# Performance work log

Measured on AMD Instinct MI355X. Metric: run time of the kernel, lower is better.

The kernel has to match this reference:

```python
import jax, jax.numpy as jnp
import numpy as np

N = 16000; E = 256000; K = 4000; H = 4; D = 128; CL = 16
NODE_VOCAB = 512; TASK_VOCAB = 128; NEG = 0.2


def _gat_sparse(h_in, src, dst, W, a_s, a_d, b):
    # PyG GATConv, heads=H, concat=False, eval mode (attention dropout off)
    n = h_in.shape[0]
    h = (h_in @ W.T).reshape(n, H, D)                       # [N,H,D]
    e = jax.nn.leaky_relu((h * a_s).sum(-1)[src] + (h * a_d).sum(-1)[dst], NEG)  # [E,H]
    emax = jax.ops.segment_max(e, dst, num_segments=n)
    ex = jnp.exp(e - emax[dst])
    den = jax.ops.segment_sum(ex, dst, num_segments=n)
    alpha = ex / (den[dst] + 1e-16)                         # edge softmax over dst
    out = jax.ops.segment_sum(h[src] * alpha[:, :, None], dst, num_segments=n)
    return out.mean(axis=1) + b                             # mean over heads + bias


def reference(x, edge_index, batch, task, node_emb, task_emb,
              W1, as1, ad1, b1, W2, as2, ad2, b2, W3, as3, ad3, b3,
              sag_wrel, sag_brel, sag_wroot, dmon_w, dmon_b,
              Wt, att_s_t, att_d_t, bt, gate_w, gate_b, trans_w, trans_b,
              task_w, task_b, fuse_w, fuse_b, out_w, out_b):
    src0, dst0 = edge_index[0], edge_index[1]
    loops = jnp.arange(N, dtype=src0.dtype)                 # GATConv add_self_loops=True
    src = jnp.concatenate([src0, loops]); dst = jnp.concatenate([dst0, loops])
    h = node_emb[x]
    h = jax.nn.relu(_gat_sparse(h, src, dst, W1, as1, ad1, b1))
    h = jax.nn.relu(_gat_sparse(h, src, dst, W2, as2, ad2, b2))
    h = jax.nn.relu(_gat_sparse(h, src, dst, W3, as3, ad3, b3))
    # SAGPooling: GraphConv score (add-aggr) + top-k (single graph, k=K), tanh gating
    agg = jax.ops.segment_sum(h[src0], dst0, num_segments=N)
    score = (agg @ sag_wrel.T + sag_brel + h @ sag_wroot.T)[:, 0]
    vals, perm = jax.lax.top_k(score, K)
    xp = h[perm] * jnp.tanh(vals)[:, None]                  # [K,D]
    # filter_adj + to_dense_adj: dense [K,K] adjacency among kept nodes (adj[src,dst]+=1)
    new_idx = jnp.full((N,), -1, jnp.int32).at[perm].set(jnp.arange(K, dtype=jnp.int32))
    ni, nj = new_idx[src0], new_idx[dst0]
    valid = (ni >= 0) & (nj >= 0)
    adj = jnp.zeros((K + 1, K + 1), xp.dtype).at[
        jnp.where(valid, ni, K), jnp.where(valid, nj, K)].add(1.0)[:K, :K]
    dx, adj = xp[None], adj[None]                           # [1,K,D], [1,K,K]; mask all-true
    # DMoNPooling
    s = jax.nn.softmax(dx @ dmon_w.T + dmon_b, axis=-1)     # [1,K,CL]
    out_x = jax.nn.selu(jnp.einsum('bnc,bnf->bcf', s, dx))  # [1,CL,D]
    out_adj = jnp.einsum('bnc,bnm,bmd->bcd', s, adj, s)     # [1,CL,CL]
    deg = adj.sum(axis=1)[..., None]                        # einsum('ijk->ik'): [1,K,1]
    m = deg.sum(axis=(1, 2)) / 2
    ca = jnp.einsum('bnc,bnl->bcl', s, deg)                 # [1,CL,1]
    cb = jnp.einsum('bln,bnc->blc', jnp.swapaxes(deg, 1, 2), s)  # [1,1,CL]
    spectral = (-jnp.trace(out_adj - ca @ cb / 2 / m[:, None, None], axis1=1, axis2=2) / 2 / m).mean()
    ss = jnp.einsum('bnc,bnd->bcd', s, s)
    i_s = jnp.eye(CL, dtype=ss.dtype)
    ortho = jnp.linalg.norm(ss / jnp.linalg.norm(ss, axis=(1, 2), keepdims=True)
                            - i_s / jnp.sqrt(jnp.asarray(CL, ss.dtype)), axis=(1, 2)).mean()
    cluster = (jnp.linalg.norm(s.sum(axis=1), axis=1) / K * jnp.sqrt(jnp.asarray(CL, ss.dtype)) - 1).mean()
    gp_loss = spectral + ortho + cluster
    out_adj = out_adj * (1.0 - i_s)                         # zero diagonal
    ds = jnp.sqrt(out_adj.sum(axis=2)) + 1e-15              # [1,CL]
    out_adj = out_adj / ds[:, None, :] / ds[:, :, None]
    # DenseGATConv (add_loop=True sets diag to 1; adj only used as a mask)
    hh = (out_x @ Wt.T).reshape(1, CL, H, D)
    al = jax.nn.leaky_relu((hh * att_s_t).sum(-1)[:, None, :, :]
                           + (hh * att_d_t).sum(-1)[:, :, None, :], NEG)  # [1,i,j,H]
    adj_l = out_adj * (1.0 - i_s) + i_s
    al = jnp.where(adj_l[..., None] == 0, -jnp.inf, al)
    al = jax.nn.softmax(al, axis=2)
    dg = jax.nn.relu(jnp.einsum('bijh,bjhd->bihd', al, hh).mean(axis=2) + bt)  # [1,CL,D]
    # gated readout (DenseAggregation)
    gate = jax.nn.softmax((dg @ gate_w.T + gate_b)[..., 0], axis=-1)           # [1,CL]
    ro = jnp.einsum('bn,bnd->bd', gate, dg @ trans_w.T + trans_b)              # [1,D]
    te = jax.nn.relu(task_emb[task] @ task_w.T + task_b)                       # [1,D]
    fuse = jax.nn.relu(jnp.concatenate([ro, te], axis=-1) @ fuse_w.T + fuse_b)
    out = fuse @ out_w.T + out_b                                               # [1,1]
    return out, gp_loss


def setup_inputs() -> dict:
    key = jax.random.key(0)
    ks = iter(jax.random.split(key, 64))
    def nrm(shape, scale=0.05):
        return jax.random.normal(next(ks), shape, jnp.float32) * scale
    inp = {}
    inp['x'] = jax.random.randint(next(ks), (N,), 0, NODE_VOCAB, dtype=jnp.int32)
    src = jax.random.randint(next(ks), (E,), 0, N, dtype=jnp.int32)
    off = jax.random.randint(next(ks), (E,), 1, N, dtype=jnp.int32)
    inp['edge_index'] = jnp.stack([src, (src + off) % N])  # no self-loops
    inp['batch'] = jnp.zeros((N,), jnp.int32)
    inp['task'] = jax.random.randint(next(ks), (1,), 0, TASK_VOCAB, dtype=jnp.int32)
    inp['node_emb'] = nrm((NODE_VOCAB, D), D ** -0.5)
    inp['task_emb'] = nrm((TASK_VOCAB, D), D ** -0.5)
    for i in (1, 2, 3):
        inp[f'W{i}'] = nrm((H * D, D)); inp[f'as{i}'] = nrm((H, D))
        inp[f'ad{i}'] = nrm((H, D)); inp[f'b{i}'] = jnp.zeros((D,), jnp.float32)
    inp['sag_wrel'] = nrm((1, D)); inp['sag_brel'] = jnp.zeros((1,), jnp.float32)
    inp['sag_wroot'] = nrm((1, D))
    inp['dmon_w'] = nrm((CL, D)); inp['dmon_b'] = jnp.zeros((CL,), jnp.float32)
    inp['Wt'] = nrm((H * D, D)); inp['att_s_t'] = nrm((H, D)); inp['att_d_t'] = nrm((H, D))
    inp['bt'] = jnp.zeros((D,), jnp.float32)
    inp['gate_w'] = nrm((1, D)); inp['gate_b'] = jnp.zeros((1,), jnp.float32)
    inp['trans_w'] = nrm((D, D)); inp['trans_b'] = jnp.zeros((D,), jnp.float32)
    inp['task_w'] = nrm((D, D)); inp['task_b'] = jnp.zeros((D,), jnp.float32)
    inp['fuse_w'] = nrm((D, 2 * D)); inp['fuse_b'] = jnp.zeros((D,), jnp.float32)
    inp['out_w'] = nrm((1, D)); inp['out_b'] = jnp.zeros((1,), jnp.float32)
    return inp
```

## Files before the change

### kernel.cpp

```cpp
#include <hip/hip_runtime.h>
#include <hip/hip_bf16.h>
#include <math.h>

constexpr int NN  = 16000;
constexpr int NE  = 256000;
constexpr int NET = NE + NN;
constexpr int NK  = 4000;
constexpr int NH  = 4;
constexpr int ND  = 128;
constexpr int NCL = 16;

constexpr int A_ADJ    = 0;
constexpr int A_SS     = 256;
constexpr int A_CSUM   = 512;
constexpr int A_V      = 528;
constexpr int A_DEGSUM = 544;
constexpr int A_OUTX   = 560;
constexpr int A_ADJN   = 2608;
constexpr int ACC_FLOATS = 3072;

typedef short sh8 __attribute__((ext_vector_type(8)));
typedef float f32x4 __attribute__((ext_vector_type(4)));

__device__ inline unsigned fkey(float f){
  unsigned u = __float_as_uint(f);
  return (u & 0x80000000u) ? ~u : (u | 0x80000000u);
}

__device__ inline unsigned short f2bf(float f){
  unsigned u = __float_as_uint(f);
  unsigned r = u + 0x7FFFu + ((u>>16)&1u);
  return (unsigned short)(r>>16);
}

__device__ inline float bflo(unsigned v){ return __uint_as_float(v<<16); }
__device__ inline float bfhi(unsigned v){ return __uint_as_float(v & 0xFFFF0000u); }

__global__ void k_init(int* cnt, int* node2k, float* tbuf, float* deg, float* acc,
                       const float* __restrict__ dw, unsigned short* __restrict__ dwb){
  int i = blockIdx.x*blockDim.x + threadIdx.x;
  int stride = gridDim.x*blockDim.x;
  for (int j=i; j<NN; j+=stride){ cnt[j]=0; node2k[j]=-1; }
  for (int j=i; j<NK*NCL; j+=stride) tbuf[j]=0.f;
  for (int j=i; j<NK; j+=stride) deg[j]=0.f;
  for (int j=i; j<ACC_FLOATS; j+=stride) acc[j]=0.f;
  if (blockIdx.x==0){
    int idx = threadIdx.x;
    int kc = idx>>6, lane = idx&63;
    int c = lane&15, q = lane>>4;
    sh8 v;
    #pragma unroll
    for (int j=0;j<8;j++) v[j] = (short)f2bf(dw[(size_t)c*128 + kc*32 + q*8 + j]);
    ((sh8*)dwb)[idx] = v;
  }
}

__global__ void k_count(const int* __restrict__ ei, int* __restrict__ cnt){
  int e = blockIdx.x*blockDim.x + threadIdx.x;
  if (e >= NET) return;
  int d = (e < NE) ? ei[NE+e] : (e-NE);
  atomicAdd(&cnt[d], 1);
}

__global__ __launch_bounds__(1024) void k_scan(int* cnt, int* ptr, int* fill){
  __shared__ int sums[1024];
  int t = threadIdx.x;
  constexpr int PER = 16;
  int base = t*PER;
  int v[PER];
  int run = 0;
  #pragma unroll
  for (int i=0;i<PER;i++){
    int idx = base+i;
    int c = (idx<NN)? cnt[idx] : 0;
    v[i] = run; run += c;
  }
  sums[t] = run;
  __syncthreads();
  for (int o=1;o<1024;o<<=1){
    int add = (t>=o)? sums[t-o] : 0;
    __syncthreads();
    sums[t] += add;
    __syncthreads();
  }
  int ex = sums[t] - run;
  #pragma unroll
  for (int i=0;i<PER;i++){
    int idx = base+i;
    if (idx<NN){ int p = ex+v[i]; ptr[idx]=p; fill[idx]=p; }
  }
  if (t==1023) ptr[NN]=sums[1023];
}

__global__ void k_fill(const int* __restrict__ ei, int* cur, int* csrc){
  int e = blockIdx.x*blockDim.x + threadIdx.x;
  if (e >= NET) return;
  int s, d;
  if (e < NE){ s = ei[e]; d = ei[NE+e]; } else { s = e-NE; d = e-NE; }
  int pos = atomicAdd(&cur[d], 1);
  csrc[pos] = s;
}

__global__ void k_embed(const int* __restrict__ x, const float* __restrict__ emb,
                        unsigned short* __restrict__ hbf){
  int i = blockIdx.x*blockDim.x + threadIdx.x;
  if (i >= NN*32) return;
  int n = i >> 5, q = i & 31;
  float4 v = ((const float4*)emb)[(size_t)x[n]*32 + q];
  ushort4 b;
  b.x = f2bf(v.x); b.y = f2bf(v.y); b.z = f2bf(v.z); b.w = f2bf(v.w);
  ((ushort4*)hbf)[i] = b;
}

__global__ __launch_bounds__(256) void k_prepc(const float* __restrict__ W,
                                               const float* __restrict__ as_,
                                               const float* __restrict__ ad_,
                                               float* __restrict__ usd,
                                               unsigned short* __restrict__ Blay){
  int b = blockIdx.x;
  if (b < 32){
    int idx = b*256 + threadIdx.x;
    int lane = idx&63, kc = (idx>>6)&15, c = idx>>10;
    int d = c*16 + (lane&15), q = lane>>4;
    sh8 v;
    #pragma unroll
    for (int j=0;j<8;j++){
      int kkg = kc*32 + q*8 + j;
      int h = kkg>>7, k = kkg&127;
      v[j] = (short)f2bf(W[(size_t)(h*128+d)*128 + k]);
    }
    *((sh8*)(Blay + (size_t)idx*8)) = v;
  } else {
    for (int t = threadIdx.x; t < 512; t += 256){
      int h = t>>7, k = t&127;
      float ss=0.f, sd=0.f;
      for (int d=0; d<128; d++){
        float w = W[(size_t)(h*128+d)*128 + k];
        ss += as_[h*128+d]*w;
        sd += ad_[h*128+d]*w;
      }
      usd[t] = ss;
      usd[512+t] = sd;
    }
  }
}

__global__ __launch_bounds__(64) void k_attnsum(const unsigned short* __restrict__ hbf,
                          const float* __restrict__ usd,
                          float* __restrict__ sum_s, float* __restrict__ sum_d){
  int n = blockIdx.x, lane = threadIdx.x;
  unsigned hv = *(const unsigned*)&hbf[(size_t)n*128 + 2*lane];
  float x0 = bflo(hv), x1 = bfhi(hv);
  #pragma unroll
  for (int h=0;h<4;h++){
    float2 us = *(const float2*)&usd[h*128 + 2*lane];
    float2 ud = *(const float2*)&usd[512 + h*128 + 2*lane];
    float ps = x0*us.x + x1*us.y;
    float pd = x0*ud.x + x1*ud.y;
    #pragma unroll
    for (int off=32; off>0; off>>=1){ ps += __shfl_down(ps,off); pd += __shfl_down(pd,off); }
    if (lane==0){ sum_s[n*4+h]=ps; sum_d[n*4+h]=pd; }
  }
}

__global__ __launch_bounds__(64) void k_edgesw(const int* __restrict__ ptr,
                        const int* __restrict__ csrc,
                        const float* __restrict__ sum_s, const float* __restrict__ sum_d,
                        unsigned short* __restrict__ alphab){
  int n = blockIdx.x; int lane = threadIdx.x;
  int b0 = ptr[n], b1 = ptr[n+1];
  int deg = b1 - b0;
  float4 sd = ((const float4*)sum_d)[n];
  int j0 = b0 + lane;
  bool act = lane < deg;
  float vx=-1e30f, vy=-1e30f, vz=-1e30f, vw=-1e30f;
  if (act){
    float4 ss = ((const float4*)sum_s)[csrc[j0]];
    vx = ss.x+sd.x; vx = vx>0.f? vx : 0.2f*vx;
    vy = ss.y+sd.y; vy = vy>0.f? vy : 0.2f*vy;
    vz = ss.z+sd.z; vz = vz>0.f? vz : 0.2f*vz;
    vw = ss.w+sd.w; vw = vw>0.f? vw : 0.2f*vw;
  }
  float mx=vx, my=vy, mz=vz, mw=vw;
  for (int base=64; base<deg; base+=64){
    int j = b0+base+lane;
    if (j<b1){
      float4 ss = ((const float4*)sum_s)[csrc[j]];
      float t0=ss.x+sd.x; t0=t0>0.f?t0:0.2f*t0; mx=fmaxf(mx,t0);
      float t1=ss.y+sd.y; t1=t1>0.f?t1:0.2f*t1; my=fmaxf(my,t1);
      float t2=ss.z+sd.z; t2=t2>0.f?t2:0.2f*t2; mz=fmaxf(mz,t2);
      float t3=ss.w+sd.w; t3=t3>0.f?t3:0.2f*t3; mw=fmaxf(mw,t3);
    }
  }
  #pragma unroll
  for (int o=1;o<64;o<<=1){
    mx=fmaxf(mx,__shfl_xor(mx,o)); my=fmaxf(my,__shfl_xor(my,o));
    mz=fmaxf(mz,__shfl_xor(mz,o)); mw=fmaxf(mw,__shfl_xor(mw,o));
  }
  float dx = act? __expf(vx-mx):0.f, dy = act? __expf(vy-my):0.f;
  float dz = act? __expf(vz-mz):0.f, dw = act? __expf(vw-mw):0.f;
  for (int base=64; base<deg; base+=64){
    int j = b0+base+lane;
    if (j<b1){
      float4 ss = ((const float4*)sum_s)[csrc[j]];
      float t0=ss.x+sd.x; t0=t0>0.f?t0:0.2f*t0; dx+=__expf(t0-mx);
      float t1=ss.y+sd.y; t1=t1>0.f?t1:0.2f*t1; dy+=__expf(t1-my);
      float t2=ss.z+sd.z; t2=t2>0.f?t2:0.2f*t2; dz+=__expf(t2-mz);
      float t3=ss.w+sd.w; t3=t3>0.f?t3:0.2f*t3; dw+=__expf(t3-mw);
    }
  }
  #pragma unroll
  for (int o=1;o<64;o<<=1){
    dx+=__shfl_xor(dx,o); dy+=__shfl_xor(dy,o);
    dz+=__shfl_xor(dz,o); dw+=__shfl_xor(dw,o);
  }
  float scx = 0.25f/(dx+1e-16f), scy = 0.25f/(dy+1e-16f);
  float scz = 0.25f/(dz+1e-16f), scw = 0.25f/(dw+1e-16f);
  if (act){
    ushort4 o4;
    o4.x = f2bf(__expf(vx-mx)*scx); o4.y = f2bf(__expf(vy-my)*scy);
    o4.z = f2bf(__expf(vz-mz)*scz); o4.w = f2bf(__expf(vw-mw)*scw);
    *(ushort4*)&alphab[(size_t)j0*4] = o4;
  }
  for (int base=64; base<deg; base+=64){
    int j = b0+base+lane;
    if (j<b1){
      float4 ss = ((const float4*)sum_s)[csrc[j]];
      float t0=ss.x+sd.x; t0=t0>0.f?t0:0.2f*t0;
      float t1=ss.y+sd.y; t1=t1>0.f?t1:0.2f*t1;
      float t2=ss.z+sd.z; t2=t2>0.f?t2:0.2f*t2;
      float t3=ss.w+sd.w; t3=t3>0.f?t3:0.2f*t3;
      ushort4 o4;
      o4.x=f2bf(__expf(t0-mx)*scx); o4.y=f2bf(__expf(t1-my)*scy);
      o4.z=f2bf(__expf(t2-mz)*scz); o4.w=f2bf(__expf(t3-mw)*scw);
      *(ushort4*)&alphab[(size_t)j*4] = o4;
    }
  }
}

__global__ __launch_bounds__(64) void k_agg(const int* __restrict__ ptr,
                      const int* __restrict__ csrc,
                      const unsigned short* __restrict__ alphab,
                      const unsigned short* __restrict__ hbf,
                      unsigned short* __restrict__ agg){
  int n = blockIdx.x; int t = threadIdx.x;
  int b0 = ptr[n], b1 = ptr[n+1];
  float a00=0.f,a01=0.f,a10=0.f,a11=0.f,a20=0.f,a21=0.f,a30=0.f,a31=0.f;
  for (int j=b0;j<b1;j++){
    int s = csrc[j];
    uint2 al = *(const uint2*)&alphab[(size_t)j*4];
    float ax = bflo(al.x), ay = bfhi(al.x);
    float az = bflo(al.y), aw = bfhi(al.y);
    unsigned hv = *(const unsigned*)&hbf[(size_t)s*128 + 2*t];
    float v0 = bflo(hv), v1 = bfhi(hv);
    a00 += ax*v0; a01 += ax*v1;
    a10 += ay*v0; a11 += ay*v1;
    a20 += az*v0; a21 += az*v1;
    a30 += aw*v0; a31 += aw*v1;
  }
  unsigned short* o = agg + (size_t)n*512;
  *(ushort2*)&o[      2*t] = (ushort2){f2bf(a00), f2bf(a01)};
  *(ushort2*)&o[128 + 2*t] = (ushort2){f2bf(a10), f2bf(a11)};
  *(ushort2*)&o[256 + 2*t] = (ushort2){f2bf(a20), f2bf(a21)};
  *(ushort2*)&o[384 + 2*t] = (ushort2){f2bf(a30), f2bf(a31)};
}

__global__ __launch_bounds__(256) void k_gemmb(const unsigned short* __restrict__ A,
                                               const unsigned short* __restrict__ B,
                                               const float* __restrict__ bias,
                                               float* __restrict__ C,
                                               unsigned short* __restrict__ Cb,
                                               int writeF32){
  int tid = threadIdx.x;
  int w = tid>>6, lane = tid&63;
  int m0 = blockIdx.x*64 + w*16;
  int quad = lane>>4;
  int mrow = m0 + (lane&15);
  const sh8* arow = (const sh8*)(A + (size_t)mrow*512 + quad*8);
  sh8 af[16];
  #pragma unroll
  for (int kc=0;kc<16;kc++) af[kc] = arow[kc*4];
  f32x4 acc[8];
  #pragma unroll
  for (int c=0;c<8;c++) acc[c] = (f32x4){0.f,0.f,0.f,0.f};
  const sh8* bp = (const sh8*)B;
  #pragma unroll
  for (int kc=0;kc<16;kc++){
    #pragma unroll
    for (int c=0;c<8;c++){
      sh8 bf = bp[(c*16+kc)*64 + lane];
      acc[c] = __builtin_amdgcn_mfma_f32_16x16x32_bf16(af[kc], bf, acc[c], 0, 0, 0);
    }
  }
  #pragma unroll
  for (int c=0;c<8;c++){
    int d = c*16 + (lane&15);
    float bi = bias[d];
    #pragma unroll
    for (int r=0;r<4;r++){
      int m = m0 + quad*4 + r;
      float v = fmaxf(acc[c][r] + bi, 0.f);
      Cb[(size_t)m*128 + d] = f2bf(v);
      if (writeF32) C[(size_t)m*128 + d] = v;
    }
  }
}

__global__ __launch_bounds__(64) void k_pq(const float* __restrict__ h,
                     const float* __restrict__ wrel,
                     const float* __restrict__ wroot, float* __restrict__ p,
                     float* __restrict__ q){
  int n = blockIdx.x; int lane = threadIdx.x;
  const float* row = h+(size_t)n*128;
  float a = row[lane]*wrel[lane] + row[64+lane]*wrel[64+lane];
  float b = row[lane]*wroot[lane] + row[64+lane]*wroot[64+lane];
  #pragma unroll
  for (int o=32;o>0;o>>=1){ a += __shfl_down(a,o); b += __shfl_down(b,o); }
  if (lane==0){ p[n]=a; q[n]=b; }
}

__global__ __launch_bounds__(64) void k_sagw(const int* __restrict__ ptr,
                           const int* __restrict__ csrc,
                           const float* __restrict__ p, const float* __restrict__ q,
                           const float* __restrict__ brel, float* __restrict__ score){
  int n = blockIdx.x; int lane = threadIdx.x;
  int b0=ptr[n], b1=ptr[n+1];
  float s=0.f;
  for (int j=b0+lane; j<b1; j+=64){
    int sj=csrc[j];
    if (sj!=n) s+=p[sj];
  }
  #pragma unroll
  for (int o=32;o>0;o>>=1) s += __shfl_down(s,o);
  if (lane==0) score[n] = s + q[n] + brel[0];
}

__global__ __launch_bounds__(1024) void k_topk(const float* __restrict__ score,
                                               int* __restrict__ sel){
  __shared__ int hist[8*257];
  __shared__ int hmerge[256];
  __shared__ unsigned sh_prefix;
  __shared__ int sh_rem;
  __shared__ int cntGT, cntEQ;
  __shared__ int ties[256];
  int t = threadIdx.x;
  int lane = t & 63;
  int rep = t >> 7;
  unsigned keys[16];
  #pragma unroll
  for (int j=0;j<16;j++){
    int i = t + j*1024;
    keys[j] = (i<NN) ? fkey(score[i]) : 0u;
  }
  if (t==0){ sh_prefix=0u; sh_rem=NK; cntGT=0; cntEQ=0; }
  __syncthreads();
  for (int p=0;p<4;p++){
    int shift = 24-8*p;
    for (int i=t;i<8*257;i+=1024) hist[i]=0;
    __syncthreads();
    unsigned prefix = sh_prefix;
    #pragma unroll
    for (int j=0;j<16;j++){
      bool val = (j<15) || (t < (NN - 15*1024));
      unsigned u = keys[j];
      bool ok = val && ((p==0) || ((u>>(shift+8)) == (prefix>>(shift+8))));
      int b = (int)((u>>shift)&255u);
      unsigned long long act = __ballot(ok);
      if (act){
        int leader = (int)(__ffsll((long long)act)-1);
        int bl = __shfl(b, leader);
        unsigned long long same = __ballot(ok && b==bl);
        if (same==act){
          if (lane==leader) atomicAdd(&hist[rep*257+bl], (int)__popcll(act));
        } else if (ok){
          atomicAdd(&hist[rep*257+b], 1);
        }
      }
    }
    __syncthreads();
    if (t<256){
      int v=0;
      #pragma unroll
      for (int r=0;r<8;r++) v += hist[r*257+t];
      hmerge[t]=v;
    }
    __syncthreads();
    if (t<64){
      int l = t;
      int b0 = 4*(63-l);
      int c3 = hmerge[b0+3], c2 = hmerge[b0+2], c1 = hmerge[b0+1], c0 = hmerge[b0];
      int gs = c0+c1+c2+c3;
      int incl = gs;
      #pragma unroll
      for (int o=1;o<64;o<<=1){
        int v = __shfl_up(incl, o);
        if (l>=o) incl += v;
      }
      int excl = incl - gs;
      int rem = sh_rem;
      int rl = rem - excl;
      if (rl > 0 && rl <= gs){
// ... 102 lines not shown
      float sm = e;
      #pragma unroll
      for (int o=1;o<16;o<<=1) sm += __shfl_xor(sm, o);
      sA[(size_t)(k0+quad*4+r)*16 + col] = e/sm;
    }
  }
}

__global__ void k_edgepool(const int* __restrict__ ei, const int* __restrict__ node2k,
                           const float* __restrict__ sA, float* __restrict__ tbuf,
                           float* __restrict__ deg){
  int e = blockIdx.x*blockDim.x + threadIdx.x;
  if (e >= NE) return;
  int ni = node2k[ei[e]];
  int nj = node2k[ei[NE+e]];
  if (ni >= 0 && nj >= 0){
    atomicAdd(&deg[nj], 1.f);
    const float* sr = &sA[(size_t)nj*16];
    float* tr = &tbuf[(size_t)ni*16];
    #pragma unroll
    for (int c=0;c<16;c++) atomicAdd(&tr[c], sr[c]);
  }
}

constexpr int P_BLOCKS = 80;
constexpr int P_ROWS   = NK / P_BLOCKS;
constexpr int P_CHUNK  = 25;

__global__ __launch_bounds__(256) void k_pool(const float* __restrict__ sA,
                                              const float* __restrict__ xp,
                                              const float* __restrict__ tb,
                                              const float* __restrict__ deg,
                                              float* __restrict__ acc){
  __shared__ float sv[P_CHUNK*16];
  __shared__ float tv[P_CHUNK*16];
  __shared__ float dv[P_CHUNK];
  __shared__ float xv[P_CHUNK*128];
  int t = threadIdx.x;
  int c = t>>4, d = t&15;
  float loc[8] = {0,0,0,0,0,0,0,0};
  float a_adj=0.f, a_ss=0.f, a_cs=0.f, a_v=0.f, a_dg=0.f;
  int r0 = blockIdx.x*P_ROWS;
  for (int ch=0; ch<P_ROWS; ch+=P_CHUNK){
    int base = r0+ch;
    for (int i=t;i<P_CHUNK*16;i+=256){
      sv[i] = sA[(size_t)(base+(i>>4))*16 + (i&15)];
      tv[i] = tb[(size_t)(base+(i>>4))*16 + (i&15)];
    }
    for (int i=t;i<P_CHUNK*128;i+=256)
      xv[i] = xp[(size_t)(base+(i>>7))*128 + (i&127)];
    if (t<P_CHUNK) dv[t]=deg[base+t];
    __syncthreads();
    for (int r=0;r<P_CHUNK;r++){
      float sc = sv[r*16+c];
      a_adj += sc*tv[r*16+d];
      a_ss  += sc*sv[r*16+d];
      if (d==0){ a_cs += sc; a_v += sc*dv[r]; }
      if (t==0) a_dg += dv[r];
      #pragma unroll
      for (int j=0;j<8;j++){
        int o=t+j*256;
        loc[j] += sv[r*16+(o>>7)]*xv[r*128+(o&127)];
      }
    }
    __syncthreads();
  }
  atomicAdd(&acc[A_ADJ + t], a_adj);
  atomicAdd(&acc[A_SS + t], a_ss);
  if (d==0){ atomicAdd(&acc[A_CSUM+c], a_cs); atomicAdd(&acc[A_V+c], a_v); }
  if (t==0) atomicAdd(&acc[A_DEGSUM], a_dg);
  #pragma unroll
  for (int j=0;j<8;j++) atomicAdd(&acc[A_OUTX + t + j*256], loc[j]);
}

__device__ float block_sum_256(float v, float* red){
  int t = threadIdx.x;
  red[t]=v; __syncthreads();
  #pragma unroll
  for (int o=128;o>0;o>>=1){ if (t<o) red[t]+=red[t+o]; __syncthreads(); }
  float r = red[0]; __syncthreads();
  return r;
}

__global__ __launch_bounds__(256) void k_finloss(float* __restrict__ acc, float* __restrict__ dout){
  __shared__ float red[256];
  __shared__ float dsv[16];
  int t = threadIdx.x;
  int c = t>>4, dcol = t&15;
  float m = 0.5f*acc[A_DEGSUM];
  float ssv = acc[A_SS+t];
  float tr    = block_sum_256((t<16)? acc[A_ADJ + t*16 + t] : 0.f, red);
  float sumv2 = block_sum_256((t<16)? acc[A_V+t]*acc[A_V+t] : 0.f, red);
  float ss2   = block_sum_256(ssv*ssv, red);
  float cs2   = block_sum_256((t<16)? acc[A_CSUM+t]*acc[A_CSUM+t] : 0.f, red);
  float ssn = sqrtf(ss2);
  float term = ssv/ssn - ((c==dcol)? 0.25f : 0.f);
  float ortho2 = block_sum_256(term*term, red);
  if (t==0){
    float spectral = -(tr - sumv2/(2.f*m))/(2.f*m);
    float ortho = sqrtf(ortho2);
    float cluster = sqrtf(cs2)/(float)NK*4.f - 1.f;
    dout[1] = spectral + ortho + cluster;
  }
  float z = (c==dcol)? 0.f : acc[A_ADJ+t];
  red[t]=z; __syncthreads();
  for (int o=8;o>0;o>>=1){ if (dcol<o) red[t]+=red[t+o]; __syncthreads(); }
  if (dcol==0) dsv[c]=sqrtf(red[c*16])+1e-15f;
  __syncthreads();
  acc[A_ADJN+t] = z/(dsv[c]*dsv[dcol]);
  #pragma unroll
  for (int j=0;j<8;j++){
    int idx = t + j*256;
    float xv = acc[A_OUTX+idx];
    float s2 = (xv > 0.f)? xv : 1.6732632423543772f*expm1f(xv);
    acc[A_OUTX+idx] = 1.0507009873554805f*s2;
  }
}

__global__ void k_hh(const float* __restrict__ acc, const float* __restrict__ Wt,
                     float* __restrict__ hh){
  int of = blockIdx.x*256 + threadIdx.x;
  int c = of >> 9, o = of & 511;
  const float* sx = acc + A_OUTX + c*128;
  const float* w = Wt + (size_t)o*128;
  float s=0.f;
  for (int k=0;k<128;k++) s += sx[k]*w[k];
  hh[of] = s;
}

__global__ __launch_bounds__(256) void k_head(
    const float* __restrict__ hh_g, const float* __restrict__ acc,
    const float* __restrict__ att_s, const float* __restrict__ att_d,
    const float* __restrict__ bt, const float* __restrict__ gate_w,
    const float* __restrict__ gate_b, const float* __restrict__ trans_w,
    const float* __restrict__ trans_b, const int* __restrict__ task,
    const float* __restrict__ task_emb, const float* __restrict__ task_w,
    const float* __restrict__ task_b, const float* __restrict__ fuse_w,
    const float* __restrict__ fuse_b, const float* __restrict__ out_w,
    const float* __restrict__ out_b, float* __restrict__ dout){
  __shared__ float hh[8192];
  __shared__ float al[1024];
  __shared__ float asrc[64], adst[64];
  __shared__ float dg[2048];
  __shared__ float gate[16];
  __shared__ float gvec[128];
  __shared__ float ro[128], te[128], fu[128];
  __shared__ float red[256];
  int t = threadIdx.x;
  for (int i=t;i<8192;i+=256) hh[i]=hh_g[i];
  __syncthreads();
  if (t<128){
    int j = t>>3; int h = (t>>1)&3; int w = t&1;
    const float* hr = &hh[j*512 + h*128];
    const float* a = (w? att_d : att_s) + h*128;
    float s=0.f;
    for (int k2=0;k2<128;k2++) s += hr[k2]*a[k2];
    if (w) adst[j*4+h]=s; else asrc[j*4+h]=s;
  }
  __syncthreads();
  for (int idx=t; idx<1024; idx+=256){
    int h = idx&3, j=(idx>>2)&15, i=idx>>6;
    float v = asrc[j*4+h] + adst[i*4+h];
    v = v>0.f? v : 0.2f*v;
    float adjl = (i==j)? 1.f : acc[A_ADJN + i*16+j];
    al[idx] = (adjl==0.f)? -1e30f : v;
  }
  __syncthreads();
  if (t<64){
    int i=t>>2, h=t&3;
    float mx=-1e30f;
    for (int j=0;j<16;j++) mx = fmaxf(mx, al[(i*16+j)*4+h]);
    float sum=0.f;
    for (int j=0;j<16;j++){ float e=__expf(al[(i*16+j)*4+h]-mx); al[(i*16+j)*4+h]=e; sum+=e; }
    float inv = 1.f/sum;
    for (int j=0;j<16;j++) al[(i*16+j)*4+h]*=inv;
  }
  __syncthreads();
  for (int idx=t; idx<2048; idx+=256){
    int i=idx>>7, d=idx&127;
    float s=0.f;
    for (int h=0;h<4;h++)
      for (int j=0;j<16;j++)
        s += al[(i*16+j)*4+h]*hh[j*512+h*128+d];
    dg[idx] = fmaxf(0.25f*s + bt[d], 0.f);
  }
  __syncthreads();
  if (t<16){
    float s=0.f;
    for (int d2=0;d2<128;d2++) s += dg[t*128+d2]*gate_w[d2];
    red[t] = s + gate_b[0];
  }
  __syncthreads();
  if (t<16){
    float mx=-1e30f; for (int i=0;i<16;i++) mx=fmaxf(mx,red[i]);
    float s=0.f; for (int i=0;i<16;i++) s+=__expf(red[i]-mx);
    gate[t]=__expf(red[t]-mx)/s;
  }
  __syncthreads();
  if (t<128){
    float s=0.f;
    for (int i=0;i<16;i++) s += gate[i]*dg[i*128+t];
    gvec[t]=s;
  }
  __syncthreads();
  if (t<128){
    float s=0.f;
    for (int k2=0;k2<128;k2++) s += gvec[k2]*trans_w[t*128+k2];
    ro[t]=s+trans_b[t];
    int tk = task[0];
    float s2=0.f;
    for (int k2=0;k2<128;k2++) s2 += task_emb[(size_t)tk*128+k2]*task_w[t*128+k2];
    te[t]=fmaxf(s2+task_b[t],0.f);
  }
  __syncthreads();
  if (t<128){
    float s=0.f;
    for (int k2=0;k2<128;k2++) s += ro[k2]*fuse_w[t*256+k2] + te[k2]*fuse_w[t*256+128+k2];
    fu[t]=fmaxf(s+fuse_b[t],0.f);
  }
  __syncthreads();
  float v = (t<128)? fu[t]*out_w[t] : 0.f;
  red[t]=v; __syncthreads();
  for (int o=128;o>0;o>>=1){ if (t<o) red[t]+=red[t+o]; __syncthreads(); }
  if (t==0) dout[0]=red[0]+out_b[0];
}

extern "C" void kernel_launch(void* const* d_in, const int* in_sizes, int n_in,
                              void* d_out, int out_size, void* d_ws, size_t ws_size,
                              hipStream_t stream){
  const int* x        = (const int*)d_in[0];
  const int* ei       = (const int*)d_in[1];
  const int* task     = (const int*)d_in[3];
  const float* node_emb = (const float*)d_in[4];
  const float* task_emb = (const float*)d_in[5];
  const float* W[3]  = {(const float*)d_in[6],  (const float*)d_in[10], (const float*)d_in[14]};
  const float* As_[3]= {(const float*)d_in[7],  (const float*)d_in[11], (const float*)d_in[15]};
  const float* Ad_[3]= {(const float*)d_in[8],  (const float*)d_in[12], (const float*)d_in[16]};
  const float* Bb[3] = {(const float*)d_in[9],  (const float*)d_in[13], (const float*)d_in[17]};
  const float* wrel  = (const float*)d_in[18];
  const float* brel  = (const float*)d_in[19];
  const float* wroot = (const float*)d_in[20];
  const float* dmon_w= (const float*)d_in[21];
  const float* dmon_b= (const float*)d_in[22];
  const float* Wt    = (const float*)d_in[23];
  const float* att_s = (const float*)d_in[24];
  const float* att_d = (const float*)d_in[25];
  const float* btb   = (const float*)d_in[26];
  const float* gate_w= (const float*)d_in[27];
  const float* gate_b= (const float*)d_in[28];
  const float* trans_w=(const float*)d_in[29];
  const float* trans_b=(const float*)d_in[30];
  const float* task_w= (const float*)d_in[31];
  const float* task_b= (const float*)d_in[32];
  const float* fuse_w= (const float*)d_in[33];
  const float* fuse_b= (const float*)d_in[34];
  const float* out_w = (const float*)d_in[35];
  const float* out_b = (const float*)d_in[36];
  float* dout = (float*)d_out;
  (void)in_sizes; (void)n_in; (void)out_size; (void)ws_size;

  char* base = (char*)d_ws;
  size_t off = 0;
  auto alloc = [&](size_t bytes)->char*{
    off = (off + 255) & ~(size_t)255;
    char* r = base + off; off += bytes; return r;
  };
  int* csr_ptr  = (int*)alloc((size_t)(NN+1)*4);
  int* csr_fill = (int*)alloc((size_t)NN*4);
  int* csr_src  = (int*)alloc((size_t)NET*4);
  int* sel      = (int*)alloc((size_t)NK*4);
  int* node2k   = (int*)alloc((size_t)NN*4);
  float* score  = (float*)alloc((size_t)NN*4);
  float* pbuf   = (float*)alloc((size_t)NN*4);
  float* qbuf   = (float*)alloc((size_t)NN*4);
  float* h_a    = (float*)alloc((size_t)NN*128*4);
  unsigned short* hbf  = (unsigned short*)alloc((size_t)NN*128*2);
  unsigned short* aggb = (unsigned short*)alloc((size_t)NN*512*2);
  unsigned short* blay = (unsigned short*)alloc((size_t)8192*8*2);
  unsigned short* dwb  = (unsigned short*)alloc((size_t)256*8*2);
  float* usd    = (float*)alloc((size_t)1024*4);
  float* sum_s  = (float*)alloc((size_t)NN*4*4);
  float* sum_d  = (float*)alloc((size_t)NN*4*4);
  unsigned short* alphab = (unsigned short*)alloc((size_t)NET*4*2);
  float* xp     = (float*)alloc((size_t)NK*128*4);
  float* sA     = (float*)alloc((size_t)NK*16*4);
  float* tbuf   = (float*)alloc((size_t)NK*16*4);
  float* deg    = (float*)alloc((size_t)NK*4);
  float* acc    = (float*)alloc((size_t)ACC_FLOATS*4);
  float* hh_g   = (float*)alloc((size_t)8192*4);

  k_init<<<256, 256, 0, stream>>>(csr_fill, node2k, tbuf, deg, acc, dmon_w, dwb);
  k_count<<<(NET+255)/256, 256, 0, stream>>>(ei, csr_fill);
  k_scan<<<1, 1024, 0, stream>>>(csr_fill, csr_ptr, csr_fill);
  k_fill<<<(NET+255)/256, 256, 0, stream>>>(ei, csr_fill, csr_src);
  k_embed<<<(NN*32+255)/256, 256, 0, stream>>>(x, node_emb, hbf);

  for (int l=0;l<3;l++){
    k_prepc<<<33, 256, 0, stream>>>(W[l], As_[l], Ad_[l], usd, blay);
    k_attnsum<<<NN, 64, 0, stream>>>(hbf, usd, sum_s, sum_d);
    k_edgesw<<<NN, 64, 0, stream>>>(csr_ptr, csr_src, sum_s, sum_d, alphab);
    k_agg<<<NN, 64, 0, stream>>>(csr_ptr, csr_src, alphab, hbf, aggb);
    k_gemmb<<<NN/64, 256, 0, stream>>>(aggb, blay, Bb[l], h_a, hbf, (l==2)?1:0);
  }
  k_pq<<<NN, 64, 0, stream>>>(h_a, wrel, wroot, pbuf, qbuf);
  k_sagw<<<NN, 64, 0, stream>>>(csr_ptr, csr_src, pbuf, qbuf, brel, score);
  k_topk<<<1, 1024, 0, stream>>>(score, sel);
  k_gassign<<<NK/16, 256, 0, stream>>>(sel, score, h_a, xp, node2k, dwb, dmon_b, sA);
  k_edgepool<<<(NE+255)/256, 256, 0, stream>>>(ei, node2k, sA, tbuf, deg);
  k_pool<<<P_BLOCKS, 256, 0, stream>>>(sA, xp, tbuf, deg, acc);
  k_finloss<<<1, 256, 0, stream>>>(acc, dout);
  k_hh<<<32, 256, 0, stream>>>(acc, Wt, hh_g);
  k_head<<<1, 256, 0, stream>>>(hh_g, acc, att_s, att_d, btb, gate_w, gate_b,
                                trans_w, trans_b, task, task_emb, task_w, task_b,
                                fuse_w, fuse_b, out_w, out_b, dout);
}
```

Baseline: 515.1 us.

## Fuse GAT stages: edge softmax with aggregation, attention sums into GEMM epilogue

Several independent fusions at once. Per-layer weight prep for all three layers moves into the init kernel. The embedding gather is merged with the attention-sum computation. Edge softmax and neighbor aggregation share one kernel, with alphas kept in shared memory, so the bf16 alpha buffer round trip is gone. The next layer's attention sums and the SAG p/q projections are computed in the GEMM epilogue, and the finloss/hh/head tail kernels become one single-block kernel. The aim is fewer launches and less global traffic, at the cost of a serial Wt matvec inside one block and more work per edge-aggregation block.

```diff
diff --git a/kernel.cpp b/kernel.cpp
--- a/kernel.cpp
+++ b/kernel.cpp
@@ -6,8 +6,6 @@
 constexpr int NE  = 256000;
 constexpr int NET = NE + NN;
 constexpr int NK  = 4000;
-constexpr int NH  = 4;
-constexpr int ND  = 128;
 constexpr int NCL = 16;
 
 constexpr int A_ADJ    = 0;
@@ -16,7 +14,6 @@
 constexpr int A_V      = 528;
 constexpr int A_DEGSUM = 544;
 constexpr int A_OUTX   = 560;
-constexpr int A_ADJN   = 2608;
 constexpr int ACC_FLOATS = 3072;
 
 typedef short sh8 __attribute__((ext_vector_type(8)));
@@ -26,25 +23,62 @@
   unsigned u = __float_as_uint(f);
   return (u & 0x80000000u) ? ~u : (u | 0x80000000u);
 }
-
 __device__ inline unsigned short f2bf(float f){
   unsigned u = __float_as_uint(f);
   unsigned r = u + 0x7FFFu + ((u>>16)&1u);
   return (unsigned short)(r>>16);
 }
-
 __device__ inline float bflo(unsigned v){ return __uint_as_float(v<<16); }
 __device__ inline float bfhi(unsigned v){ return __uint_as_float(v & 0xFFFF0000u); }
 
-__global__ void k_init(int* cnt, int* node2k, float* tbuf, float* deg, float* acc,
-                       const float* __restrict__ dw, unsigned short* __restrict__ dwb){
+__global__ __launch_bounds__(256) void k_init(int* cnt, int* node2k, float* tbuf,
+                       float* deg, float* acc,
+                       const float* __restrict__ dw, unsigned short* __restrict__ dwb,
+                       const float* __restrict__ W0, const float* __restrict__ as0, const float* __restrict__ ad0,
+                       const float* __restrict__ W1, const float* __restrict__ as1, const float* __restrict__ ad1,
+                       const float* __restrict__ W2, const float* __restrict__ as2, const float* __restrict__ ad2,
+                       float* __restrict__ usd, unsigned short* __restrict__ Blay){
   int i = blockIdx.x*blockDim.x + threadIdx.x;
   int stride = gridDim.x*blockDim.x;
   for (int j=i; j<NN; j+=stride){ cnt[j]=0; node2k[j]=-1; }
   for (int j=i; j<NK*NCL; j+=stride) tbuf[j]=0.f;
   for (int j=i; j<NK; j+=stride) deg[j]=0.f;
   for (int j=i; j<ACC_FLOATS; j+=stride) acc[j]=0.f;
-  if (blockIdx.x==0){
+  int b = blockIdx.x;
+  const float* Wl[3] = {W0, W1, W2};
+  const float* al_s[3] = {as0, as1, as2};
+  const float* al_d[3] = {ad0, ad1, ad2};
+  if (b < 96){
+    int layer = b>>5;
+    const float* W = Wl[layer];
+    int idx = (b&31)*256 + threadIdx.x;
+    int lane = idx&63, kc = (idx>>6)&15, c = idx>>10;
+    int d = c*16 + (lane&15), q = lane>>4;
+    sh8 v;
+    #pragma unroll
+    for (int j=0;j<8;j++){
+      int kkg = kc*32 + q*8 + j;
+      int h = kkg>>7, k = kkg&127;
+      v[j] = (short)f2bf(W[(size_t)(h*128+d)*128 + k]);
+    }
+    *((sh8*)(Blay + (size_t)layer*65536 + (size_t)idx*8)) = v;
+  } else if (b < 99){
+    int layer = b-96;
+    const float* W = Wl[layer];
+    const float* as_ = al_s[layer];
+    const float* ad_ = al_d[layer];
+    for (int t2 = threadIdx.x; t2 < 512; t2 += 256){
+      int h = t2>>7, k = t2&127;
+      float ss=0.f, sd=0.f;
+      for (int d=0; d<128; d++){
+        float w = W[(size_t)(h*128+d)*128 + k];
+        ss += as_[h*128+d]*w;
+        sd += ad_[h*128+d]*w;
+      }
+      usd[layer*1024 + t2] = ss;
+      usd[layer*1024 + 512 + t2] = sd;
+    }
+  } else if (b == 99){
     int idx = threadIdx.x;
     int kc = idx>>6, lane = idx&63;
     int c = lane&15, q = lane>>4;
@@ -101,81 +135,49 @@
   csrc[pos] = s;
 }
 
-__global__ void k_embed(const int* __restrict__ x, const float* __restrict__ emb,
-                        unsigned short* __restrict__ hbf){
-  int i = blockIdx.x*blockDim.x + threadIdx.x;
-  if (i >= NN*32) return;
-  int n = i >> 5, q = i & 31;
-  float4 v = ((const float4*)emb)[(size_t)x[n]*32 + q];
-  ushort4 b;
-  b.x = f2bf(v.x); b.y = f2bf(v.y); b.z = f2bf(v.z); b.w = f2bf(v.w);
-  ((ushort4*)hbf)[i] = b;
-}
-
-__global__ __launch_bounds__(256) void k_prepc(const float* __restrict__ W,
-                                               const float* __restrict__ as_,
-                                               const float* __restrict__ ad_,
-                                               float* __restrict__ usd,
-                                               unsigned short* __restrict__ Blay){
-  int b = blockIdx.x;
-  if (b < 32){
-    int idx = b*256 + threadIdx.x;
-    int lane = idx&63, kc = (idx>>6)&15, c = idx>>10;
-    int d = c*16 + (lane&15), q = lane>>4;
-    sh8 v;
-    #pragma unroll
-    for (int j=0;j<8;j++){
-      int kkg = kc*32 + q*8 + j;
-      int h = kkg>>7, k = kkg&127;
-      v[j] = (short)f2bf(W[(size_t)(h*128+d)*128 + k]);
-    }
-    *((sh8*)(Blay + (size_t)idx*8)) = v;
-  } else {
-    for (int t = threadIdx.x; t < 512; t += 256){
-      int h = t>>7, k = t&127;
-      float ss=0.f, sd=0.f;
-      for (int d=0; d<128; d++){
-        float w = W[(size_t)(h*128+d)*128 + k];
-        ss += as_[h*128+d]*w;
-        sd += ad_[h*128+d]*w;
-      }
-      usd[t] = ss;
-      usd[512+t] = sd;
-    }
-  }
-}
-
-__global__ __launch_bounds__(64) void k_attnsum(const unsigned short* __restrict__ hbf,
-                          const float* __restrict__ usd,
-                          float* __restrict__ sum_s, float* __restrict__ sum_d){
+__global__ __launch_bounds__(64) void k_embsum(const int* __restrict__ x,
+    const float* __restrict__ emb, const float* __restrict__ usd,
+    unsigned short* __restrict__ hbf, float* __restrict__ sum_s,
+    float* __restrict__ sum_d){
   int n = blockIdx.x, lane = threadIdx.x;
-  unsigned hv = *(const unsigned*)&hbf[(size_t)n*128 + 2*lane];
-  float x0 = bflo(hv), x1 = bfhi(hv);
+  int xv = x[n];
+  float2 v = *(const float2*)&emb[(size_t)xv*128 + 2*lane];
+  *(ushort2*)&hbf[(size_t)n*128 + 2*lane] = (ushort2){f2bf(v.x), f2bf(v.y)};
+  float ps[4], pd[4];
   #pragma unroll
   for (int h=0;h<4;h++){
     float2 us = *(const float2*)&usd[h*128 + 2*lane];
     float2 ud = *(const float2*)&usd[512 + h*128 + 2*lane];
-    float ps = x0*us.x + x1*us.y;
-    float pd = x0*ud.x + x1*ud.y;
-    #pragma unroll
-    for (int off=32; off>0; off>>=1){ ps += __shfl_down(ps,off); pd += __shfl_down(pd,off); }
-    if (lane==0){ sum_s[n*4+h]=ps; sum_d[n*4+h]=pd; }
-  }
-}
-
-__global__ __launch_bounds__(64) void k_edgesw(const int* __restrict__ ptr,
-                        const int* __restrict__ csrc,
-                        const float* __restrict__ sum_s, const float* __restrict__ sum_d,
-                        unsigned short* __restrict__ alphab){
+    ps[h] = v.x*us.x + v.y*us.y;
+    pd[h] = v.x*ud.x + v.y*ud.y;
+  }
+  #pragma unroll
+  for (int o=32;o>0;o>>=1){
+    #pragma unroll
+    for (int h=0;h<4;h++){ ps[h]+=__shfl_down(ps[h],o); pd[h]+=__shfl_down(pd[h],o); }
+  }
+  if (lane==0){
+    ((float4*)sum_s)[n] = (float4){ps[0],ps[1],ps[2],ps[3]};
+    ((float4*)sum_d)[n] = (float4){pd[0],pd[1],pd[2],pd[3]};
+  }
+}
+
+__global__ __launch_bounds__(64) void k_edgeagg(const int* __restrict__ ptr,
+    const int* __restrict__ csrc,
+    const float* __restrict__ sum_s, const float* __restrict__ sum_d,
+    const unsigned short* __restrict__ hbf, unsigned short* __restrict__ agg){
+  __shared__ float alf[64*4];
+  __shared__ int   sN[64];
   int n = blockIdx.x; int lane = threadIdx.x;
   int b0 = ptr[n], b1 = ptr[n+1];
   int deg = b1 - b0;
   float4 sd = ((const float4*)sum_d)[n];
-  int j0 = b0 + lane;
   bool act = lane < deg;
+  int s0i = -1;
   float vx=-1e30f, vy=-1e30f, vz=-1e30f, vw=-1e30f;
   if (act){
-    float4 ss = ((const float4*)sum_s)[csrc[j0]];
+    s0i = csrc[b0+lane];
+    float4 ss = ((const float4*)sum_s)[s0i];
     vx = ss.x+sd.x; vx = vx>0.f? vx : 0.2f*vx;
     vy = ss.y+sd.y; vy = vy>0.f? vy : 0.2f*vy;
     vz = ss.z+sd.z; vz = vz>0.f? vz : 0.2f*vz;
@@ -216,66 +218,85 @@
   }
   float scx = 0.25f/(dx+1e-16f), scy = 0.25f/(dy+1e-16f);
   float scz = 0.25f/(dz+1e-16f), scw = 0.25f/(dw+1e-16f);
-  if (act){
-    ushort4 o4;
-    o4.x = f2bf(__expf(vx-mx)*scx); o4.y = f2bf(__expf(vy-my)*scy);
-    o4.z = f2bf(__expf(vz-mz)*scz); o4.w = f2bf(__expf(vw-mw)*scw);
-    *(ushort4*)&alphab[(size_t)j0*4] = o4;
-  }
-  for (int base=64; base<deg; base+=64){
-    int j = b0+base+lane;
-    if (j<b1){
-      float4 ss = ((const float4*)sum_s)[csrc[j]];
-      float t0=ss.x+sd.x; t0=t0>0.f?t0:0.2f*t0;
-      float t1=ss.y+sd.y; t1=t1>0.f?t1:0.2f*t1;
-      float t2=ss.z+sd.z; t2=t2>0.f?t2:0.2f*t2;
-      float t3=ss.w+sd.w; t3=t3>0.f?t3:0.2f*t3;
-      ushort4 o4;
-      o4.x=f2bf(__expf(t0-mx)*scx); o4.y=f2bf(__expf(t1-my)*scy);
-      o4.z=f2bf(__expf(t2-mz)*scz); o4.w=f2bf(__expf(t3-mw)*scw);
-      *(ushort4*)&alphab[(size_t)j*4] = o4;
-    }
-  }
-}
-
-__global__ __launch_bounds__(64) void k_agg(const int* __restrict__ ptr,
-                      const int* __restrict__ csrc,
-                      const unsigned short* __restrict__ alphab,
-                      const unsigned short* __restrict__ hbf,
-                      unsigned short* __restrict__ agg){
-  int n = blockIdx.x; int t = threadIdx.x;
-  int b0 = ptr[n], b1 = ptr[n+1];
   float a00=0.f,a01=0.f,a10=0.f,a11=0.f,a20=0.f,a21=0.f,a30=0.f,a31=0.f;
-  for (int j=b0;j<b1;j++){
-    int s = csrc[j];
-    uint2 al = *(const uint2*)&alphab[(size_t)j*4];
-    float ax = bflo(al.x), ay = bfhi(al.x);
-    float az = bflo(al.y), aw = bfhi(al.y);
-    unsigned hv = *(const unsigned*)&hbf[(size_t)s*128 + 2*t];
-    float v0 = bflo(hv), v1 = bfhi(hv);
-    a00 += ax*v0; a01 += ax*v1;
-    a10 += ay*v0; a11 += ay*v1;
-    a20 += az*v0; a21 += az*v1;
-    a30 += aw*v0; a31 += aw*v1;
+  for (int base=0; base<deg; base+=64){
+    if (base){
+      __syncthreads();
+      int j = b0+base+lane;
+      if (j<b1){
+        s0i = csrc[j];
+        float4 ss = ((const float4*)sum_s)[s0i];
+        vx=ss.x+sd.x; vx=vx>0.f?vx:0.2f*vx;
+        vy=ss.y+sd.y; vy=vy>0.f?vy:0.2f*vy;
+        vz=ss.z+sd.z; vz=vz>0.f?vz:0.2f*vz;
+        vw=ss.w+sd.w; vw=vw>0.f?vw:0.2f*vw;
+      }
+    }
+    if (base+lane < deg){
+      alf[lane*4+0]=__expf(vx-mx)*scx; alf[lane*4+1]=__expf(vy-my)*scy;
+      alf[lane*4+2]=__expf(vz-mz)*scz; alf[lane*4+3]=__expf(vw-mw)*scw;
+      sN[lane]=s0i;
+    }
+    __syncthreads();
+    int m = deg-base; if (m>64) m=64;
+    int e=0;
+    for (; e+4<=m; e+=4){
+      int t0=sN[e], t1=sN[e+1], t2=sN[e+2], t3=sN[e+3];
+      float4 A0=*(float4*)&alf[e*4],   A1=*(float4*)&alf[e*4+4];
+      float4 A2=*(float4*)&alf[e*4+8], A3=*(float4*)&alf[e*4+12];
+      unsigned g0=*(const unsigned*)&hbf[(size_t)t0*128+2*lane];
+      unsigned g1=*(const unsigned*)&hbf[(size_t)t1*128+2*lane];
+      unsigned g2=*(const unsigned*)&hbf[(size_t)t2*128+2*lane];
+      unsigned g3=*(const unsigned*)&hbf[(size_t)t3*128+2*lane];
+      float p0=bflo(g0), p1=bfhi(g0);
+      a00+=A0.x*p0; a01+=A0.x*p1; a10+=A0.y*p0; a11+=A0.y*p1;
+      a20+=A0.z*p0; a21+=A0.z*p1; a30+=A0.w*p0; a31+=A0.w*p1;
+      p0=bflo(g1); p1=bfhi(g1);
+      a00+=A1.x*p0; a01+=A1.x*p1; a10+=A1.y*p0; a11+=A1.y*p1;
+      a20+=A1.z*p0; a21+=A1.z*p1; a30+=A1.w*p0; a31+=A1.w*p1;
+      p0=bflo(g2); p1=bfhi(g2);
+      a00+=A2.x*p0; a01+=A2.x*p1; a10+=A2.y*p0; a11+=A2.y*p1;
+      a20+=A2.z*p0; a21+=A2.z*p1; a30+=A2.w*p0; a31+=A2.w*p1;
+      p0=bflo(g3); p1=bfhi(g3);
+      a00+=A3.x*p0; a01+=A3.x*p1; a10+=A3.y*p0; a11+=A3.y*p1;
+      a20+=A3.z*p0; a21+=A3.z*p1; a30+=A3.w*p0; a31+=A3.w*p1;
+    }
+    for (; e<m; e++){
+      int t0=sN[e];
+      float4 A0=*(float4*)&alf[e*4];
+      unsigned g0=*(const unsigned*)&hbf[(size_t)t0*128+2*lane];
+      float p0=bflo(g0), p1=bfhi(g0);
+      a00+=A0.x*p0; a01+=A0.x*p1; a10+=A0.y*p0; a11+=A0.y*p1;
+      a20+=A0.z*p0; a21+=A0.z*p1; a30+=A0.w*p0; a31+=A0.w*p1;
+    }
   }
   unsigned short* o = agg + (size_t)n*512;
-  *(ushort2*)&o[      2*t] = (ushort2){f2bf(a00), f2bf(a01)};
-  *(ushort2*)&o[128 + 2*t] = (ushort2){f2bf(a10), f2bf(a11)};
-  *(ushort2*)&o[256 + 2*t] = (ushort2){f2bf(a20), f2bf(a21)};
-  *(ushort2*)&o[384 + 2*t] = (ushort2){f2bf(a30), f2bf(a31)};
+  *(ushort2*)&o[      2*lane] = (ushort2){f2bf(a00), f2bf(a01)};
+  *(ushort2*)&o[128 + 2*lane] = (ushort2){f2bf(a10), f2bf(a11)};
+  *(ushort2*)&o[256 + 2*lane] = (ushort2){f2bf(a20), f2bf(a21)};
+  *(ushort2*)&o[384 + 2*lane] = (ushort2){f2bf(a30), f2bf(a31)};
 }
 
 __global__ __launch_bounds__(256) void k_gemmb(const unsigned short* __restrict__ A,
-                                               const unsigned short* __restrict__ B,
-                                               const float* __restrict__ bias,
-                                               float* __restrict__ C,
-                                               unsigned short* __restrict__ Cb,
-                                               int writeF32){
+      const unsigned short* __restrict__ B, const float* __restrict__ bias,
+      float* __restrict__ C, unsigned short* __restrict__ Cb, int writeF32,
+      int mode, const float* __restrict__ usdn,
+      const float* __restrict__ wrel, const float* __restrict__ wroot,
+      float* __restrict__ sum_s, float* __restrict__ sum_d,
+      float* __restrict__ pbuf, float* __restrict__ qbuf){
+  __shared__ float U[1024];
   int tid = threadIdx.x;
+  if (mode==0){
+    for (int i=tid;i<1024;i+=256) U[i]=usdn[i];
+  } else {
+    if (tid<128) U[tid]=wrel[tid];
+    else if (tid<256) U[tid]=wroot[tid-128];
+  }
+  __syncthreads();
   int w = tid>>6, lane = tid&63;
   int m0 = blockIdx.x*64 + w*16;
-  int quad = lane>>4;
-  int mrow = m0 + (lane&15);
+  int quad = lane>>4, col16 = lane&15;
+  int mrow = m0 + col16;
   const sh8* arow = (const sh8*)(A + (size_t)mrow*512 + quad*8);
   sh8 af[16];
   #pragma unroll
@@ -292,31 +313,49 @@
       acc[c] = __builtin_amdgcn_mfma_f32_16x16x32_bf16(af[kc], bf, acc[c], 0, 0, 0);
     }
   }
-  #pragma unroll
-  for (int c=0;c<8;c++){
-    int d = c*16 + (lane&15);
-    float bi = bias[d];
-    #pragma unroll
-    for (int r=0;r<4;r++){
-      int m = m0 + quad*4 + r;
-      float v = fmaxf(acc[c][r] + bi, 0.f);
-      Cb[(size_t)m*128 + d] = f2bf(v);
-      if (writeF32) C[(size_t)m*128 + d] = v;
-    }
-  }
-}
-
-__global__ __launch_bounds__(64) void k_pq(const float* __restrict__ h,
-                     const float* __restrict__ wrel,
-                     const float* __restrict__ wroot, float* __restrict__ p,
-                     float* __restrict__ q){
-  int n = blockIdx.x; int lane = threadIdx.x;
-  const float* row = h+(size_t)n*128;
-  float a = row[lane]*wrel[lane] + row[64+lane]*wrel[64+lane];
-  float b = row[lane]*wroot[lane] + row[64+lane]*wroot[64+lane];
-  #pragma unroll
-  for (int o=32;o>0;o>>=1){ a += __shfl_down(a,o); b += __shfl_down(b,o); }
-  if (lane==0){ p[n]=a; q[n]=b; }
+  float br[8];
+  #pragma unroll
+  for (int c=0;c<8;c++) br[c] = bias[c*16+col16];
+  #pragma unroll
+  for (int r=0;r<4;r++){
+    int m = m0 + quad*4 + r;
+    float vv[8];
+    #pragma unroll
+    for (int c=0;c<8;c++){
+      vv[c] = fmaxf(acc[c][r] + br[c], 0.f);
+      Cb[(size_t)m*128 + c*16+col16] = f2bf(vv[c]);
+      if (writeF32) C[(size_t)m*128 + c*16+col16] = vv[c];
+    }
+    if (mode==0){
+      float p0=0,p1=0,p2=0,p3=0,q0=0,q1=0,q2=0,q3=0;
+      #pragma unroll
+      for (int c=0;c<8;c++){
+        int o = c*16+col16;
+        float val = vv[c];
+        p0+=val*U[o];     p1+=val*U[128+o]; p2+=val*U[256+o]; p3+=val*U[384+o];
+        q0+=val*U[512+o]; q1+=val*U[640+o]; q2+=val*U[768+o]; q3+=val*U[896+o];
+      }
+      #pragma unroll
+      for (int o2=1;o2<16;o2<<=1){
+        p0+=__shfl_xor(p0,o2); p1+=__shfl_xor(p1,o2); p2+=__shfl_xor(p2,o2); p3+=__shfl_xor(p3,o2);
+        q0+=__shfl_xor(q0,o2); q1+=__shfl_xor(q1,o2); q2+=__shfl_xor(q2,o2); q3+=__shfl_xor(q3,o2);
+      }
+      if (col16==0){
+        ((float4*)sum_s)[m] = (float4){p0,p1,p2,p3};
+        ((float4*)sum_d)[m] = (float4){q0,q1,q2,q3};
+      }
+    } else {
+      float pp=0.f, qq=0.f;
+      #pragma unroll
+      for (int c=0;c<8;c++){
+        int o = c*16+col16;
+        pp += vv[c]*U[o]; qq += vv[c]*U[128+o];
+      }
+      #pragma unroll
+      for (int o2=1;o2<16;o2<<=1){ pp+=__shfl_xor(pp,o2); qq+=__shfl_xor(qq,o2); }
+      if (col16==0){ pbuf[m]=pp; qbuf[m]=qq; }
+    }
+  }
 }
 
 __global__ __launch_bounds__(64) void k_sagw(const int* __restrict__ ptr,
@@ -585,9 +624,27 @@
   return r;
 }
 
-__global__ __launch_bounds__(256) void k_finloss(float* __restrict__ acc, float* __restrict__ dout){
+__global__ __launch_bounds__(256) void k_tail(float* __restrict__ acc,
+    const float* __restrict__ Wt,
+    const float* __restrict__ att_s, const float* __restrict__ att_d,
+    const float* __restrict__ bt, const float* __restrict__ gate_w,
+    const float* __restrict__ gate_b, const float* __restrict__ trans_w,
+    const float* __restrict__ trans_b, const int* __restrict__ task,
+    const float* __restrict__ task_emb, const float* __restrict__ task_w,
+    const float* __restrict__ task_b, const float* __restrict__ fuse_w,
+    const float* __restrict__ fuse_b, const float* __restrict__ out_w,
+    const float* __restrict__ out_b, float* __restrict__ dout){
   __shared__ float red[256];
   __shared__ float dsv[16];
+  __shared__ float adjn[256];
+  __shared__ float sx[2048];
+  __shared__ float hh[8192];
+  __shared__ float al[1024];
+  __shared__ float asrc[64], adst[64];
+  __shared__ float dg[2048];
+  __shared__ float gate[16];
+  __shared__ float gvec[128];
+  __shared__ float ro[128], te[128], fu[128];
   int t = threadIdx.x;
   int c = t>>4, dcol = t&15;
   float m = 0.5f*acc[A_DEGSUM];
@@ -610,47 +667,27 @@
   for (int o=8;o>0;o>>=1){ if (dcol<o) red[t]+=red[t+o]; __syncthreads(); }
   if (dcol==0) dsv[c]=sqrtf(red[c*16])+1e-15f;
   __syncthreads();
-  acc[A_ADJN+t] = z/(dsv[c]*dsv[dcol]);
+  adjn[t] = z/(dsv[c]*dsv[dcol]);
   #pragma unroll
   for (int j=0;j<8;j++){
     int idx = t + j*256;
     float xv = acc[A_OUTX+idx];
     float s2 = (xv > 0.f)? xv : 1.6732632423543772f*expm1f(xv);
-    acc[A_OUTX+idx] = 1.0507009873554805f*s2;
-  }
-}
-
-__global__ void k_hh(const float* __restrict__ acc, const float* __restrict__ Wt,
-                     float* __restrict__ hh){
-  int of = blockIdx.x*256 + threadIdx.x;
-  int c = of >> 9, o = of & 511;
-  const float* sx = acc + A_OUTX + c*128;
-  const float* w = Wt + (size_t)o*128;
-  float s=0.f;
-  for (int k=0;k<128;k++) s += sx[k]*w[k];
-  hh[of] = s;
-}
-
-__global__ __launch_bounds__(256) void k_head(
-    const float* __restrict__ hh_g, const float* __restrict__ acc,
-    const float* __restrict__ att_s, const float* __restrict__ att_d,
-    const float* __restrict__ bt, const float* __restrict__ gate_w,
-    const float* __restrict__ gate_b, const float* __restrict__ trans_w,
-    const float* __restrict__ trans_b, const int* __restrict__ task,
-    const float* __restrict__ task_emb, const float* __restrict__ task_w,
-    const float* __restrict__ task_b, const float* __restrict__ fuse_w,
-    const float* __restrict__ fuse_b, const float* __restrict__ out_w,
-    const float* __restrict__ out_b, float* __restrict__ dout){
-  __shared__ float hh[8192];
-  __shared__ float al[1024];
-  __shared__ float asrc[64], adst[64];
-  __shared__ float dg[2048];
-  __shared__ float gate[16];
-  __shared__ float gvec[128];
-  __shared__ float ro[128], te[128], fu[128];
-  __shared__ float red[256];
-  int t = threadIdx.x;
-  for (int i=t;i<8192;i+=256) hh[i]=hh_g[i];
+    sx[idx] = 1.0507009873554805f*s2;
+  }
+  __syncthreads();
+  for (int of=t; of<8192; of+=256){
+    int c2 = of>>9, o = of&511;
+    const float4* w4 = (const float4*)(Wt + (size_t)o*128);
+    const float4* x4 = (const float4*)&sx[c2*128];
+    float s=0.f;
+    #pragma unroll
+    for (int k=0;k<32;k++){
+      float4 a = x4[k], b = w4[k];
+      s += a.x*b.x + a.y*b.y + a.z*b.z + a.w*b.w;
+    }
+    hh[of] = s;
+  }
   __syncthreads();
   if (t<128){
     int j = t>>3; int h = (t>>1)&3; int w = t&1;
@@ -665,7 +702,7 @@
     int h = idx&3, j=(idx>>2)&15, i=idx>>6;
     float v = asrc[j*4+h] + adst[i*4+h];
     v = v>0.f? v : 0.2f*v;
-    float adjl = (i==j)? 1.f : acc[A_ADJN + i*16+j];
+    float adjl = (i==j)? 1.f : adjn[i*16+j];
     al[idx] = (adjl==0.f)? -1e30f : v;
   }
   __syncthreads();
@@ -779,41 +816,45 @@
   float* h_a    = (float*)alloc((size_t)NN*128*4);
   unsigned short* hbf  = (unsigned short*)alloc((size_t)NN*128*2);
   unsigned short* aggb = (unsigned short*)alloc((size_t)NN*512*2);
-  unsigned short* blay = (unsigned short*)alloc((size_t)8192*8*2);
+  unsigned short* blay = (unsigned short*)alloc((size_t)3*65536*2);
   unsigned short* dwb  = (unsigned short*)alloc((size_t)256*8*2);
-  float* usd    = (float*)alloc((size_t)1024*4);
+  float* usd    = (float*)alloc((size_t)3*1024*4);
   float* sum_s  = (float*)alloc((size_t)NN*4*4);
   float* sum_d  = (float*)alloc((size_t)NN*4*4);
-  unsigned short* alphab = (unsigned short*)alloc((size_t)NET*4*2);
   float* xp     = (float*)alloc((size_t)NK*128*4);
   float* sA     = (float*)alloc((size_t)NK*16*4);
   float* tbuf   = (float*)alloc((size_t)NK*16*4);
   float* deg    = (float*)alloc((size_t)NK*4);
   float* acc    = (float*)alloc((size_t)ACC_FLOATS*4);
-  float* hh_g   = (float*)alloc((size_t)8192*4);
-
-  k_init<<<256, 256, 0, stream>>>(csr_fill, node2k, tbuf, deg, acc, dmon_w, dwb);
+
+  k_init<<<256, 256, 0, stream>>>(csr_fill, node2k, tbuf, deg, acc, dmon_w, dwb,
+                                  W[0], As_[0], Ad_[0], W[1], As_[1], Ad_[1],
+                                  W[2], As_[2], Ad_[2], usd, blay);
   k_count<<<(NET+255)/256, 256, 0, stream>>>(ei, csr_fill);
   k_scan<<<1, 1024, 0, stream>>>(csr_fill, csr_ptr, csr_fill);
   k_fill<<<(NET+255)/256, 256, 0, stream>>>(ei, csr_fill, csr_src);
-  k_embed<<<(NN*32+255)/256, 256, 0, stream>>>(x, node_emb, hbf);
+  k_embsum<<<NN, 64, 0, stream>>>(x, node_emb, usd, hbf, sum_s, sum_d);
 
   for (int l=0;l<3;l++){
-    k_prepc<<<33, 256, 0, stream>>>(W[l], As_[l], Ad_[l], usd, blay);
-    k_attnsum<<<NN, 64, 0, stream>>>(hbf, usd, sum_s, sum_d);
-    k_edgesw<<<NN, 64, 0, stream>>>(csr_ptr, csr_src, sum_s, sum_d, alphab);
-    k_agg<<<NN, 64, 0, stream>>>(csr_ptr, csr_src, alphab, hbf, aggb);
-    k_gemmb<<<NN/64, 256, 0, stream>>>(aggb, blay, Bb[l], h_a, hbf, (l==2)?1:0);
-  }
-  k_pq<<<NN, 64, 0, stream>>>(h_a, wrel, wroot, pbuf, qbuf);
+    k_edgeagg<<<NN, 64, 0, stream>>>(csr_ptr, csr_src, sum_s, sum_d, hbf, aggb);
+    if (l<2){
+      k_gemmb<<<NN/64, 256, 0, stream>>>(aggb, blay + (size_t)l*65536, Bb[l],
+                                         h_a, hbf, 0, 0, usd + (l+1)*1024,
+                                         nullptr, nullptr, sum_s, sum_d,
+                                         nullptr, nullptr);
+    } else {
+      k_gemmb<<<NN/64, 256, 0, stream>>>(aggb, blay + (size_t)2*65536, Bb[2],
+                                         h_a, hbf, 1, 1, nullptr,
+                                         wrel, wroot, nullptr, nullptr,
+                                         pbuf, qbuf);
+    }
+  }
   k_sagw<<<NN, 64, 0, stream>>>(csr_ptr, csr_src, pbuf, qbuf, brel, score);
   k_topk<<<1, 1024, 0, stream>>>(score, sel);
   k_gassign<<<NK/16, 256, 0, stream>>>(sel, score, h_a, xp, node2k, dwb, dmon_b, sA);
   k_edgepool<<<(NE+255)/256, 256, 0, stream>>>(ei, node2k, sA, tbuf, deg);
   k_pool<<<P_BLOCKS, 256, 0, stream>>>(sA, xp, tbuf, deg, acc);
-  k_finloss<<<1, 256, 0, stream>>>(acc, dout);
-  k_hh<<<32, 256, 0, stream>>>(acc, Wt, hh_g);
-  k_head<<<1, 256, 0, stream>>>(hh_g, acc, att_s, att_d, btb, gate_w, gate_b,
+  k_tail<<<1, 256, 0, stream>>>(acc, Wt, att_s, att_d, btb, gate_w, gate_b,
                                 trans_w, trans_b, task, task_emb, task_w, task_b,
                                 fuse_w, fuse_b, out_w, out_b, dout);
 }
```

Measured after the change: 526.7 us. 2.2% more time.
